# Kernel optimization log

Hardware: AMD Instinct MI355X
Metric: run time of the kernel (lower is better)

## Reference

```python
import jax, jax.numpy as jnp
import numpy as np

STRIDE = 4
N_LAYERS = 4
N_HEADS = 8
D_MODEL = 1024
D_FF = 4096
WINDOW = 400 // STRIDE      # lookback window (in folded frames)
LOOKFWD = 80 // STRIDE      # lookforward (in folded frames)
ROPE_BASE = 10000.0


def _layernorm(x, scale, bias, eps=1e-5):
    mu = jnp.mean(x, axis=-1, keepdims=True)
    var = jnp.mean(jnp.square(x - mu), axis=-1, keepdims=True)
    return (x - mu) * jax.lax.rsqrt(var + eps) * scale + bias


def _rope(x):
    # x: [B, H, S, Dh]
    B, H, S, Dh = x.shape
    half = Dh // 2
    inv_freq = 1.0 / (ROPE_BASE ** (jnp.arange(half, dtype=jnp.float32) / half))
    ang = jnp.arange(S, dtype=jnp.float32)[:, None] * inv_freq[None, :]  # [S, half]
    cos = jnp.cos(ang).astype(x.dtype)
    sin = jnp.sin(ang).astype(x.dtype)
    x1, x2 = x[..., :half], x[..., half:]
    return jnp.concatenate([x1 * cos - x2 * sin, x1 * sin + x2 * cos], axis=-1)


def setup_inputs() -> dict:
    key = jax.random.key(0)
    ks = jax.random.split(key, 32)
    B, T, C = 4, 4096, 512
    L, D, F = N_LAYERS, D_MODEL, D_FF
    s = 0.02
    inp = {
        'x': jax.random.normal(ks[0], (B, T, C), dtype=jnp.float32),
        'x_lengths': jax.random.randint(ks[1], (B,), 0, T + 1, dtype=jnp.int64 if jax.config.jax_enable_x64 else jnp.int32),
        'Wp': jax.random.normal(ks[2], (C * STRIDE, D), dtype=jnp.float32) * s,
        'bp': jnp.zeros((D,), jnp.float32),
        'ln1_s': jnp.ones((L, D), jnp.float32), 'ln1_b': jnp.zeros((L, D), jnp.float32),
        'Wq': jax.random.normal(ks[3], (L, D, D), jnp.float32) * s, 'bq': jnp.zeros((L, D), jnp.float32),
        'Wk': jax.random.normal(ks[4], (L, D, D), jnp.float32) * s, 'bk': jnp.zeros((L, D), jnp.float32),
        'Wv': jax.random.normal(ks[5], (L, D, D), jnp.float32) * s, 'bv': jnp.zeros((L, D), jnp.float32),
        'Wo': jax.random.normal(ks[6], (L, D, D), jnp.float32) * s, 'bo': jnp.zeros((L, D), jnp.float32),
        'ln2_s': jnp.ones((L, D), jnp.float32), 'ln2_b': jnp.zeros((L, D), jnp.float32),
        'W1': jax.random.normal(ks[7], (L, D, F), jnp.float32) * s, 'b1': jnp.zeros((L, F), jnp.float32),
        'W2': jax.random.normal(ks[8], (L, F, D), jnp.float32) * s, 'b2': jnp.zeros((L, D), jnp.float32),
        'lnf_s': jnp.ones((D,), jnp.float32), 'lnf_b': jnp.zeros((D,), jnp.float32),
    }
    return inp


def reference(x, x_lengths, Wp, bp, ln1_s, ln1_b, Wq, bq, Wk, bk, Wv, bv, Wo, bo,
              ln2_s, ln2_b, W1, b1, W2, b2, lnf_s, lnf_b):
    B, T, C = x.shape
    S = T // STRIDE
    H, Dh = N_HEADS, D_MODEL // N_HEADS
    # stride-fold + input projection
    xf = x[:, :S * STRIDE].reshape(B, S, C * STRIDE)
    h = xf @ Wp + bp                                  # [B, S, D]
    lens = x_lengths // STRIDE
    pad = (jnp.arange(S)[None, :] < lens[:, None])    # [B, S] valid-key mask
    h = h * pad[:, :, None].astype(h.dtype)
    # sliding-window causal-with-lookforward mask + key padding
    i = jnp.arange(S)[:, None]
    j = jnp.arange(S)[None, :]
    win = (j - i <= LOOKFWD) & (i - j < WINDOW)       # [S, S]
    allowed = win[None, None] & pad[:, None, None, :] # [B, 1, S, S]
    bias = jnp.where(allowed, 0.0, -1e9).astype(h.dtype)
    scale = 1.0 / jnp.sqrt(jnp.asarray(Dh, h.dtype))
    for l in range(N_LAYERS):
        # --- pre-LN RoPE windowed attention ---
        y = _layernorm(h, ln1_s[l], ln1_b[l])
        q = (y @ Wq[l] + bq[l]).reshape(B, S, H, Dh).transpose(0, 2, 1, 3)
        k = (y @ Wk[l] + bk[l]).reshape(B, S, H, Dh).transpose(0, 2, 1, 3)
        v = (y @ Wv[l] + bv[l]).reshape(B, S, H, Dh).transpose(0, 2, 1, 3)
        q, k = _rope(q), _rope(k)
        scores = jnp.einsum('bhqe,bhke->bhqk', q, k) * scale + bias
        attn = jax.nn.softmax(scores, axis=-1)
        ctx = jnp.einsum('bhqk,bhke->bhqe', attn, v)
        ctx = ctx.transpose(0, 2, 1, 3).reshape(B, S, D_MODEL)
        h = h + ctx @ Wo[l] + bo[l]
        # --- pre-LN FFN (kernel_size=1 conv == linear), swish ---
        y = _layernorm(h, ln2_s[l], ln2_b[l])
        h = h + jax.nn.silu(y @ W1[l] + b1[l]) @ W2[l] + b2[l]
    return _layernorm(h, lnf_s, lnf_b)
```

## Files before the change

kernel.cpp:

```cpp
#include <hip/hip_runtime.h>
#include <hip/hip_bf16.h>
#include <math.h>

typedef __hip_bfloat16 bf16;
typedef __attribute__((ext_vector_type(8))) short short8;
typedef __attribute__((ext_vector_type(4))) float f32x4;

#define S_LEN 1024
#define BATCH 4
#define M_ROWS 4096
#define DMODEL 1024
#define DFF 4096
#define NHEAD 8
#define DHEAD 128
#define WIN 100
#define LFWD 20

__device__ __forceinline__ void gl_lds16(const void* g, void* l) {
    __builtin_amdgcn_global_load_lds(
        (const __attribute__((address_space(1))) void*)g,
        (__attribute__((address_space(3))) void*)l, 16, 0, 0);
}

__device__ __forceinline__ float bf2f(unsigned short u) {
    return __uint_as_float(((unsigned)u) << 16);
}

__device__ __forceinline__ int xcd_swz(int flat, int nb) {
    return (flat & 7) * (nb >> 3) + (flat >> 3);
}

template<typename TC>
__global__ __launch_bounds__(256)
void mfma_gemm(const bf16* __restrict__ A, const bf16* __restrict__ Bt,
               const float* __restrict__ bias, TC* __restrict__ C,
               int M, int N, int K, int act)
{
    __shared__ bf16 As[2][128 * 32];
    __shared__ bf16 Bs[2][128 * 32];
    const int gx = gridDim.x;
    const int nb = gx * gridDim.y;
    const int swz = xcd_swz(blockIdx.x + gx * blockIdx.y, nb);
    const int bn = (swz % gx) * 128;
    const int bm = (swz / gx) * 128;
    const int tid = threadIdx.x;
    const int w = tid >> 6, lane = tid & 63;
    const int wm = (w & 1) * 64, wn = (w >> 1) * 64;

    const int srow = w * 32 + (lane >> 2);
    const int selem = (lane & 3) * 8;
    const bf16* ga0 = A + (size_t)(bm + srow) * K + selem;
    const bf16* ga1 = ga0 + (size_t)16 * K;
    const bf16* gb0 = Bt + (size_t)(bn + srow) * K + selem;
    const bf16* gb1 = gb0 + (size_t)16 * K;
    const int l0 = (w * 32) * 32;
    const int l1 = (w * 32 + 16) * 32;

    f32x4 acc[4][4] = {};
    const int koff = (lane >> 4) * 8;
    const int fr = lane & 15;

    gl_lds16(ga0, As[0] + l0); gl_lds16(ga1, As[0] + l1);
    gl_lds16(gb0, Bs[0] + l0); gl_lds16(gb1, Bs[0] + l1);
    ga0 += 32; ga1 += 32; gb0 += 32; gb1 += 32;
    __syncthreads();

    const int nk = K >> 5;
    int cur = 0;
    for (int t = 0; t < nk; ++t) {
        if (t + 1 < nk) {
            bf16* a = As[cur ^ 1]; bf16* b = Bs[cur ^ 1];
            gl_lds16(ga0, a + l0); gl_lds16(ga1, a + l1);
            gl_lds16(gb0, b + l0); gl_lds16(gb1, b + l1);
            ga0 += 32; ga1 += 32; gb0 += 32; gb1 += 32;
        }
        short8 af[4], bfr[4];
#pragma unroll
        for (int i = 0; i < 4; ++i)
            af[i] = *(const short8*)(As[cur] + (wm + i * 16 + fr) * 32 + koff);
#pragma unroll
        for (int j = 0; j < 4; ++j)
            bfr[j] = *(const short8*)(Bs[cur] + (wn + j * 16 + fr) * 32 + koff);
#pragma unroll
        for (int i = 0; i < 4; ++i)
#pragma unroll
            for (int j = 0; j < 4; ++j)
                acc[i][j] = __builtin_amdgcn_mfma_f32_16x16x32_bf16(
                    af[i], bfr[j], acc[i][j], 0, 0, 0);
        __syncthreads();
        cur ^= 1;
    }

    const int cq = lane >> 4, cn = lane & 15;
#pragma unroll
    for (int i = 0; i < 4; ++i) {
#pragma unroll
        for (int r = 0; r < 4; ++r) {
            int row = bm + wm + i * 16 + cq * 4 + r;
#pragma unroll
            for (int j = 0; j < 4; ++j) {
                int col = bn + wn + j * 16 + cn;
                float v = acc[i][j][r] + bias[col];
                if (act) v = v / (1.0f + __expf(-v));
                C[(size_t)row * N + col] = (TC)v;
            }
        }
    }
}

__global__ __launch_bounds__(256)
void mfma_gemm_sk(const bf16* __restrict__ A, const bf16* __restrict__ Bt,
                  const float* __restrict__ bias, float* __restrict__ C,
                  const float* __restrict__ resid,
                  float* __restrict__ P0, float* __restrict__ P1, int prows0,
                  int M, int N, int K)
{
    __shared__ bf16 As[2][128 * 32];
    __shared__ bf16 Bs[2][128 * 32];
    const int gx = gridDim.x, gy = gridDim.y;
    const int nb = gx * gy * 2;
    const int swz = xcd_swz(blockIdx.x + gx * (blockIdx.y + gy * blockIdx.z), nb);
    const int bn = (swz % gx) * 128;
    const int bm = ((swz / gx) % gy) * 128;
    const int z  = swz / (gx * gy);
    const int khalf = K >> 1;
    const int kstart = z * khalf;
    const int tid = threadIdx.x;
    const int w = tid >> 6, lane = tid & 63;
    const int wm = (w & 1) * 64, wn = (w >> 1) * 64;

    const int srow = w * 32 + (lane >> 2);
    const int selem = (lane & 3) * 8;
    const bf16* ga0 = A + (size_t)(bm + srow) * K + kstart + selem;
    const bf16* ga1 = ga0 + (size_t)16 * K;
    const bf16* gb0 = Bt + (size_t)(bn + srow) * K + kstart + selem;
    const bf16* gb1 = gb0 + (size_t)16 * K;
    const int l0 = (w * 32) * 32;
    const int l1 = (w * 32 + 16) * 32;

    f32x4 acc[4][4] = {};
    const int koff = (lane >> 4) * 8;
    const int fr = lane & 15;

    gl_lds16(ga0, As[0] + l0); gl_lds16(ga1, As[0] + l1);
    gl_lds16(gb0, Bs[0] + l0); gl_lds16(gb1, Bs[0] + l1);
    ga0 += 32; ga1 += 32; gb0 += 32; gb1 += 32;
    __syncthreads();

    const int nk = khalf >> 5;
    int cur = 0;
    for (int t = 0; t < nk; ++t) {
        if (t + 1 < nk) {
            bf16* a = As[cur ^ 1]; bf16* b = Bs[cur ^ 1];
            gl_lds16(ga0, a + l0); gl_lds16(ga1, a + l1);
            gl_lds16(gb0, b + l0); gl_lds16(gb1, b + l1);
            ga0 += 32; ga1 += 32; gb0 += 32; gb1 += 32;
        }
        short8 af[4], bfr[4];
#pragma unroll
        for (int i = 0; i < 4; ++i)
            af[i] = *(const short8*)(As[cur] + (wm + i * 16 + fr) * 32 + koff);
#pragma unroll
        for (int j = 0; j < 4; ++j)
            bfr[j] = *(const short8*)(Bs[cur] + (wn + j * 16 + fr) * 32 + koff);
#pragma unroll
        for (int i = 0; i < 4; ++i)
#pragma unroll
            for (int j = 0; j < 4; ++j)
                acc[i][j] = __builtin_amdgcn_mfma_f32_16x16x32_bf16(
                    af[i], bfr[j], acc[i][j], 0, 0, 0);
        __syncthreads();
        cur ^= 1;
    }

    const int cq = lane >> 4, cn = lane & 15;
#pragma unroll
    for (int i = 0; i < 4; ++i) {
#pragma unroll
        for (int r = 0; r < 4; ++r) {
            int row = bm + wm + i * 16 + cq * 4 + r;
#pragma unroll
            for (int j = 0; j < 4; ++j) {
                int col = bn + wn + j * 16 + cn;
                float v = acc[i][j][r];
                if (z == 0) {
                    v += bias[col];
                    if (resid) v += resid[(size_t)row * N + col];
                    C[(size_t)row * N + col] = v;
                } else {
                    float* P = (row < prows0) ? (P0 + (size_t)row * N + col)
                                              : (P1 + (size_t)(row - prows0) * N + col);
                    *P = v;
                }
            }
        }
    }
}

__global__ void transpose_kernel(const float* __restrict__ W, bf16* __restrict__ Wt,
                                 int K, int N, int ld)
{
    __shared__ float t[32][33];
    const int n0 = blockIdx.x * 32, k0 = blockIdx.y * 32;
    const int tx = threadIdx.x & 31, ty = threadIdx.x >> 5;
#pragma unroll
    for (int i = 0; i < 32; i += 8)
        t[ty + i][tx] = W[(size_t)(k0 + ty + i) * ld + n0 + tx];
    __syncthreads();
#pragma unroll
    for (int i = 0; i < 32; i += 8)
        Wt[(size_t)(n0 + ty + i) * K + k0 + tx] = (bf16)t[tx][ty + i];
}

__global__ void vtrans_kernel(const bf16* __restrict__ qkv, bf16* __restrict__ vt)
{
    __shared__ bf16 t[32][33];
    const int bh = blockIdx.z;
    const int s0 = blockIdx.x * 32, d0 = blockIdx.y * 32;
    const int b = bh >> 3, h = bh & 7;
    const int tx = threadIdx.x & 31, ty = threadIdx.x >> 5;
#pragma unroll
    for (int i = 0; i < 32; i += 8)
        t[ty + i][tx] = qkv[(size_t)(b * S_LEN + s0 + ty + i) * 3072 + 2048
                            + h * DHEAD + d0 + tx];
    __syncthreads();
#pragma unroll
    for (int i = 0; i < 32; i += 8)
        vt[(size_t)(bh * DHEAD + d0 + ty + i) * 1024 + s0 + tx] = t[tx][ty + i];
}

__global__ void cvt_kernel(const float* __restrict__ s, bf16* __restrict__ d)
{
    size_t i = ((size_t)blockIdx.x * 256 + threadIdx.x) * 4;
    float4 v = *(const float4*)(s + i);
    d[i] = (bf16)v.x; d[i + 1] = (bf16)v.y; d[i + 2] = (bf16)v.z; d[i + 3] = (bf16)v.w;
}

__global__ void concat3_kernel(const float* __restrict__ a, const float* __restrict__ b,
                               const float* __restrict__ c, float* __restrict__ o)
{
    int i = blockIdx.x * 256 + threadIdx.x;
    o[i] = (i < 1024) ? a[i] : (i < 2048 ? b[i - 1024] : c[i - 2048]);
}

__global__ void pad_red_kernel(float* __restrict__ h, const float* __restrict__ P,
                               const int* __restrict__ xlen)
{
    int row = blockIdx.x;
    int b = row >> 10, s = row & 1023;
    int len = xlen[b] >> 2;
    size_t off = (size_t)row * DMODEL;
    if (s >= len) {
        for (int d = threadIdx.x; d < DMODEL; d += 256) h[off + d] = 0.0f;
    } else {
        for (int d = threadIdx.x; d < DMODEL; d += 256) h[off + d] += P[off + d];
    }
}

__global__ void reduce2_kernel(float* __restrict__ h, const float* __restrict__ P0,
                               const float* __restrict__ P1, int prows0)
{
    int row = blockIdx.x;
    const float* P = (row < prows0) ? (P0 + (size_t)row * DMODEL)
                                    : (P1 + (size_t)(row - prows0) * DMODEL);
    size_t off = (size_t)row * DMODEL;
#pragma unroll
    for (int t = 0; t < 4; ++t) {
        int d = threadIdx.x + 256 * t;
        h[off + d] += P[d];
    }
}

template<typename TO, bool RED>
__global__ void ln_kernel(float* __restrict__ x, const float* __restrict__ P0,
                          const float* __restrict__ sc, const float* __restrict__ bi,
                          TO* __restrict__ y)
{
    int row = blockIdx.x;
    float* xr = x + (size_t)row * DMODEL;
    const float* pr = RED ? (P0 + (size_t)row * DMODEL) : nullptr;
    float vals[4];
    float lsum = 0.0f, lsq = 0.0f;
#pragma unroll
    for (int t = 0; t < 4; ++t) {
        int d = threadIdx.x + 256 * t;
        float v = xr[d];
        if (RED) { v += pr[d]; xr[d] = v; }
        vals[t] = v; lsum += v; lsq += v * v;
    }
    for (int o = 32; o > 0; o >>= 1) {
        lsum += __shfl_down(lsum, o, 64);
        lsq  += __shfl_down(lsq,  o, 64);
    }
    __shared__ float s1[4], s2[4];
    int wv = threadIdx.x >> 6, ln = threadIdx.x & 63;
    if (ln == 0) { s1[wv] = lsum; s2[wv] = lsq; }
    __syncthreads();
    if (threadIdx.x == 0) {
        float a = s1[0] + s1[1] + s1[2] + s1[3];
        float b = s2[0] + s2[1] + s2[2] + s2[3];
        float mu = a * (1.0f / DMODEL);
        float var = b * (1.0f / DMODEL) - mu * mu;
        s1[0] = mu;
        s2[0] = rsqrtf(fmaxf(var, 0.0f) + 1e-5f);
    }
    __syncthreads();
    float mu = s1[0], inv = s2[0];
#pragma unroll
    for (int t = 0; t < 4; ++t) {
        int d = threadIdx.x + 256 * t;
        y[(size_t)row * DMODEL + d] = (TO)((vals[t] - mu) * inv * sc[d] + bi[d]);
    }
}

__global__ void rope_kernel(bf16* __restrict__ q, bf16* __restrict__ k, int stride)
{
    size_t idx = (size_t)blockIdx.x * 256 + threadIdx.x;
    int d = idx & 63;
    size_t rest = idx >> 6;
    int hh = rest & 7;
    int s = (rest >> 3) & 1023;
    size_t base = (rest >> 3) * stride + (size_t)hh * DHEAD;
    float inv = exp2f((float)d * -0.20762050593045235f);
    float ang = (float)s * inv;
    float c, si;
    __sincosf(ang, &si, &c);
    {
        float x1 = (float)q[base + d], x2 = (float)q[base + 64 + d];
        q[base + d]      = (bf16)(x1 * c - x2 * si);
        q[base + 64 + d] = (bf16)(x1 * si + x2 * c);
    }
    {
        float x1 = (float)k[base + d], x2 = (float)k[base + 64 + d];
        k[base + d]      = (bf16)(x1 * c - x2 * si);
        k[base + 64 + d] = (bf16)(x1 * si + x2 * c);
    }
}

__global__ void vmean_part(const bf16* __restrict__ v, float* __restrict__ part,
                           int stride)
{
    int g = blockIdx.x;
    int chunk = g & 31;
    int bh = g >> 5;
    int b = bh >> 3, hh = bh & 7;
    int d = threadIdx.x;
    const bf16* base = v + ((size_t)(b * S_LEN + chunk * 32)) * stride
                         + hh * DHEAD + d;
    float acc = 0.0f;
#pragma unroll 4
    for (int s = 0; s < 32; ++s)
        acc += (float)base[(size_t)s * stride];
    part[((size_t)bh * 32 + chunk) * DHEAD + d] = acc;
}

__global__ void vmean_fin(const float* __restrict__ part, float* __restrict__ vmean)
{
    int bh = blockIdx.x;
    int d = threadIdx.x;
    float acc = 0.0f;
#pragma unroll
    for (int c = 0; c < 32; ++c)
        acc += part[((size_t)bh * 32 + c) * DHEAD + d];
    vmean[(size_t)bh * DHEAD + d] = acc * (1.0f / S_LEN);
}

__global__ __launch_bounds__(128)
void attn_mfma(const bf16* __restrict__ qkv, const bf16* __restrict__ vt_g,
               const float* __restrict__ vmean, const int* __restrict__ xlen,
               bf16* __restrict__ ctx)
{
    __shared__ bf16 KV[2][64 * 128];
    __shared__ bf16 P[2][16 * 192];

    const int qt = blockIdx.x;
    const int bh = blockIdx.y;
    const int b = bh >> 3, h = bh & 7;
    const int tid = threadIdx.x;
    const int w = tid >> 6, l = tid & 63;
    const int qlo = qt * 32;
    const int len = xlen[b] >> 2;

    int s0 = qlo - 128; if (s0 < 0) s0 = 0;
    const int jmax = qlo + 51;
    int k0t[3]; int nt = 0;
#pragma unroll
    for (int t = 0; t < 3; ++t) {
        int k0 = s0 + t * 64;
        if (k0 <= jmax && k0 < len) { k0t[nt] = k0; ++nt; }
    }

    const bf16* qbase = qkv + (size_t)(b * S_LEN) * 3072 + h * DHEAD;
    const bf16* kbase = qbase + DMODEL;

    short8 qa[4];
    {
        const bf16* qr = qbase + (size_t)(qlo + w * 16 + (l & 15)) * 3072 + (l >> 4) * 8;
#pragma unroll
        for (int kk = 0; kk < 4; ++kk)
            qa[kk] = *(const short8*)(qr + kk * 32);
    }

    auto stageK = [&](int k0, int buf) {
#pragma unroll
        for (int c = 0; c < 8; ++c) {
            int rl = w * 32 + c * 4 + (l >> 4);
            int sr = k0 + rl; if (sr > S_LEN - 1) sr = S_LEN - 1;
            int sc = ((l & 15) * 8) ^ ((rl & 7) << 3);
            gl_lds16(kbase + (size_t)sr * 3072 + sc,
                     &KV[buf][(w * 32 + c * 4) * 128]);
        }
    };
    auto stageV = [&](int k0, int buf) {
#pragma unroll
        for (int c = 0; c < 8; ++c) {
            int d = w * 64 + c * 8 + (l >> 3);
            int js = ((l & 7) * 8) ^ ((d & 7) << 3);
            int s = k0 + js; if (s > S_LEN - 8) s = S_LEN - 8;
            gl_lds16(vt_g + (size_t)(bh * 128 + d) * 1024 + s,
                     &KV[buf][(w * 64 + c * 8) * 64]);
        }
    };

    f32x4 sf[3][4] = {};

    auto sphase = [&](int t, int buf) {
#pragma unroll
        for (int jb = 0; jb < 4; ++jb) {
            int row = jb * 16 + (l & 15);
#pragma unroll
            for (int kk = 0; kk < 4; ++kk) {
                int kel = (kk * 32 + (l >> 4) * 8) ^ ((row & 7) << 3);
                short8 kf = *(const short8*)(&KV[buf][row * 128 + kel]);
                sf[t][jb] = __builtin_amdgcn_mfma_f32_16x16x32_bf16(
                    qa[kk], kf, sf[t][jb], 0, 0, 0);
            }
        }
    };

    if (nt > 0) stageK(k0t[0], 0);
    __syncthreads();
    if (nt > 1) stageK(k0t[1], 1);
    if (nt > 0) sphase(0, 0);
    __syncthreads();
    if (nt > 2) stageK(k0t[2], 0);
    if (nt > 1) sphase(1, 1);
    __syncthreads();
    if (nt > 2) sphase(2, 0);
    if (nt > 0) stageV(k0t[0], 1);

    const float scale = 0.088388347648318447f;
    float mr[4] = {-1e30f, -1e30f, -1e30f, -1e30f};
#pragma unroll
    for (int t = 0; t < 3; ++t) if (t < nt) {
#pragma unroll
        for (int jb = 0; jb < 4; ++jb) {
            int j = k0t[t] + jb * 16 + (l & 15);
            bool jok = (j < len);
#pragma unroll
            for (int r = 0; r < 4; ++r) {
                int i = qlo + w * 16 + ((l >> 4) << 2) + r;
                float v = sf[t][jb][r] * scale;
                bool ok = jok && (j - i <= LFWD) && (i - j < WIN);
                v = ok ? v : -1e30f;
                sf[t][jb][r] = v;
                mr[r] = fmaxf(mr[r], v);
            }
        }
    }
#pragma unroll
    for (int o = 1; o <= 8; o <<= 1)
#pragma unroll
        for (int r = 0; r < 4; ++r)
            mr[r] = fmaxf(mr[r], __shfl_xor(mr[r], o, 64));

    float lr[4] = {0.0f, 0.0f, 0.0f, 0.0f};
#pragma unroll
    for (int t = 0; t < 3; ++t) if (t < nt) {
#pragma unroll
        for (int jb = 0; jb < 4; ++jb) {
#pragma unroll
            for (int r = 0; r < 4; ++r) {
                int q = ((l >> 4) << 2) + r;
                int jrel = t * 64 + jb * 16 + (l & 15);
                float e = __expf(sf[t][jb][r] - mr[r]);
                lr[r] += e;
                P[w][q * 192 + (jrel ^ ((q & 7) << 3))] = (bf16)e;
            }
        }
    }
#pragma unroll
    for (int o = 1; o <= 8; o <<= 1)
#pragma unroll
        for (int r = 0; r < 4; ++r)
            lr[r] += __shfl_xor(lr[r], o, 64);
    float inv[4];
#pragma unroll
    for (int r = 0; r < 4; ++r) inv[r] = 1.0f / fmaxf(lr[r], 1e-30f);

    __syncthreads();

    f32x4 acc[8] = {};
    auto pv = [&](int ti, int buf) {
#pragma unroll
        for (int s32 = 0; s32 < 2; ++s32) {
            int q = l & 15;
            int jr8 = ti * 64 + s32 * 32 + (l >> 4) * 8;
            short8 pa = *(const short8*)(&P[w][q * 192 + (jr8 ^ ((q & 7) << 3))]);
#pragma unroll
            for (int db = 0; db < 8; ++db) {
                int d = db * 16 + (l & 15);
                int je = (s32 * 32 + (l >> 4) * 8) ^ ((d & 7) << 3);
                short8 vf = *(const short8*)(&KV[buf][d * 64 + je]);
                acc[db] = __builtin_amdgcn_mfma_f32_16x16x32_bf16(
                    pa, vf, acc[db], 0, 0, 0);
            }
        }
    };

    if (nt > 1) stageV(k0t[1], 0);
    if (nt > 0) pv(0, 1);
    __syncthreads();
    if (nt > 2) stageV(k0t[2], 1);
    if (nt > 1) pv(1, 0);
    __syncthreads();
    if (nt > 2) pv(2, 1);

    const float* vm = vmean + (size_t)bh * DHEAD;
    float vmr[8];
#pragma unroll
    for (int db = 0; db < 8; ++db) vmr[db] = vm[db * 16 + (l & 15)];
#pragma unroll
    for (int r = 0; r < 4; ++r) {
        int i = qlo + w * 16 + ((l >> 4) << 2) + r;
        bf16* crow = ctx + (size_t)(b * S_LEN + i) * DMODEL + h * DHEAD;
        bool em = mr[r] < -1e29f;
        float iv = inv[r];
#pragma unroll
        for (int db = 0; db < 8; ++db) {
            float v = em ? vmr[db] : acc[db][r] * iv;
            crow[db * 16 + (l & 15)] = (bf16)v;
        }
    }
}

extern "C" void kernel_launch(void* const* d_in, const int* in_sizes, int n_in,
                              void* d_out, int out_size, void* d_ws, size_t ws_size,
                              hipStream_t stream)
{
    const float* x      = (const float*)d_in[0];
    const int*   xlen   = (const int*)d_in[1];
    const float* Wp     = (const float*)d_in[2];
    const float* bp     = (const float*)d_in[3];
    const float* ln1_s  = (const float*)d_in[4];
    const float* ln1_b  = (const float*)d_in[5];
    const float* Wq     = (const float*)d_in[6];
    const float* bq     = (const float*)d_in[7];
    const float* Wk     = (const float*)d_in[8];
    const float* bk     = (const float*)d_in[9];
    const float* Wv     = (const float*)d_in[10];
    const float* bv     = (const float*)d_in[11];
    const float* Wo     = (const float*)d_in[12];
    const float* bo     = (const float*)d_in[13];
    const float* ln2_s  = (const float*)d_in[14];
    const float* ln2_b  = (const float*)d_in[15];
    const float* W1     = (const float*)d_in[16];
    const float* b1     = (const float*)d_in[17];
    const float* W2     = (const float*)d_in[18];
    const float* b2     = (const float*)d_in[19];
    const float* lnf_s  = (const float*)d_in[20];
    const float* lnf_b  = (const float*)d_in[21];
    (void)in_sizes; (void)n_in; (void)out_size; (void)ws_size;

    const size_t MD = (size_t)M_ROWS * DMODEL;
    float* h     = (float*)d_ws;
    bf16*  y     = (bf16*)(h + MD);
    float* yfP   = (float*)(h + MD);
    bf16*  U     = y + MD;
    bf16*  xb    = U;
    bf16*  qkv   = U;
    bf16*  mid   = U;
    float* UfP   = (float*)U;
    float* UfP2  = (float*)(U + 8 * 1024 * 1024);
    float* vmean = (float*)(U + 16 * 1024 * 1024);
    float* bqkv  = vmean + BATCH * NHEAD * DHEAD;
    bf16*  wt    = (bf16*)d_out;
    float* doP   = (float*)((char*)d_out + 8 * 1024 * 1024);
    float* vpart = doP;
    bf16*  vt_g  = (bf16*)d_out;
    const int QS = 3 * DMODEL;

    dim3 blk(256);
    dim3 gSK(DMODEL / 128, M_ROWS / 128, 2);

    cvt_kernel<<<(2 * MD) / (256 * 4), blk, 0, stream>>>(x, xb);
    transpose_kernel<<<dim3(DMODEL / 32, 2048 / 32), blk, 0, stream>>>(Wp, wt, 2048, DMODEL, DMODEL);
    mfma_gemm_sk<<<gSK, blk, 0, stream>>>(xb, wt, bp, h, nullptr,
                                          UfP2, nullptr, M_ROWS, M_ROWS, DMODEL, 2048);
    pad_red_kernel<<<M_ROWS, blk, 0, stream>>>(h, UfP2, xlen);

    for (int l = 0; l < 4; ++l) {
        const size_t wD  = (size_t)l * DMODEL * DMODEL;
        const size_t wF  = (size_t)l * DMODEL * DFF;
        const size_t wF2 = (size_t)l * DFF * DMODEL;
        const size_t vD  = (size_t)l * DMODEL;
        const size_t vF  = (size_t)l * DFF;

        ln_kernel<bf16, false><<<M_ROWS, blk, 0, stream>>>(h, nullptr,
                                                           ln1_s + vD, ln1_b + vD, y);

        transpose_kernel<<<dim3(32, 32), blk, 0, stream>>>(Wq + wD, wt, DMODEL, DMODEL, DMODEL);
        transpose_kernel<<<dim3(32, 32), blk, 0, stream>>>(Wk + wD, wt + MD / 4, DMODEL, DMODEL, DMODEL);
        transpose_kernel<<<dim3(32, 32), blk, 0, stream>>>(Wv + wD, wt + MD / 2, DMODEL, DMODEL, DMODEL);
        concat3_kernel<<<12, blk, 0, stream>>>(bq + vD, bk + vD, bv + vD, bqkv);
        mfma_gemm<bf16><<<dim3(3 * DMODEL / 128, M_ROWS / 128), blk, 0, stream>>>(
            y, wt, bqkv, qkv, M_ROWS, 3 * DMODEL, DMODEL, 0);

        bf16* qb = qkv;
        bf16* kb = qkv + DMODEL;
        bf16* vb = qkv + 2 * DMODEL;
        rope_kernel<<<(M_ROWS * NHEAD * 64) / 256, blk, 0, stream>>>(qb, kb, QS);
        vtrans_kernel<<<dim3(32, 4, 32), blk, 0, stream>>>(qkv, vt_g);
        vmean_part<<<BATCH * NHEAD * 32, dim3(DHEAD), 0, stream>>>(vb, vpart, QS);
        vmean_fin<<<BATCH * NHEAD, dim3(DHEAD), 0, stream>>>(vpart, vmean);
        attn_mfma<<<dim3(32, 32), dim3(128), 0, stream>>>(qkv, vt_g, vmean, xlen, y);

        transpose_kernel<<<dim3(32, 32), blk, 0, stream>>>(Wo + wD, wt, DMODEL, DMODEL, DMODEL);
        mfma_gemm_sk<<<gSK, blk, 0, stream>>>(y, wt, bo + vD, h, h,
                                              UfP, nullptr, M_ROWS, M_ROWS, DMODEL, 1024);

        ln_kernel<bf16, true><<<M_ROWS, blk, 0, stream>>>(h, UfP,
                                                          ln2_s + vD, ln2_b + vD, y);

        transpose_kernel<<<dim3(DFF / 32, DMODEL / 32), blk, 0, stream>>>(
            W1 + wF, wt, DMODEL, DFF, DFF);
        mfma_gemm<bf16><<<dim3(DFF / 128, M_ROWS / 128), blk, 0, stream>>>(
            y, wt, b1 + vF, mid, M_ROWS, DFF, DMODEL, 1);

        transpose_kernel<<<dim3(DMODEL / 32, DFF / 32), blk, 0, stream>>>(
            W2 + wF2, wt, DFF, DMODEL, DMODEL);
        mfma_gemm_sk<<<gSK, blk, 0, stream>>>(mid, wt, b2 + vD, h, h,
                                              yfP, doP, 2048, M_ROWS, DMODEL, DFF);
        reduce2_kernel<<<M_ROWS, blk, 0, stream>>>(h, yfP, doP, 2048);
    }

    ln_kernel<float, false><<<M_ROWS, blk, 0, stream>>>(h, nullptr, lnf_s, lnf_b,
                                                        (float*)d_out);
}
```

Baseline: 1.466 ms.

## Triple-buffer GEMM LDS staging with explicit vmcnt waits and barriers

Both MFMA GEMM kernels move from double-buffered to triple-buffered LDS tiles. Two K-tiles are kept in flight, and precise s_waitcnt vmcnt counts decide when a tile is ready, in place of a full __syncthreads after each step. This is meant to hide more global-load latency behind the MFMA work. The cost is 48KB of LDS per block, which may lower occupancy, plus two barriers per iteration, and the code relies on hand-counted vmcnt values being correct.

```diff
diff --git a/kernel.cpp b/kernel.cpp
--- a/kernel.cpp
+++ b/kernel.cpp
@@ -16,6 +16,8 @@
 #define WIN 100
 #define LFWD 20
 
+#define SCHED0 __builtin_amdgcn_sched_barrier(0)
+
 __device__ __forceinline__ void gl_lds16(const void* g, void* l) {
     __builtin_amdgcn_global_load_lds(
         (const __attribute__((address_space(1))) void*)g,
@@ -36,8 +38,8 @@
                const float* __restrict__ bias, TC* __restrict__ C,
                int M, int N, int K, int act)
 {
-    __shared__ bf16 As[2][128 * 32];
-    __shared__ bf16 Bs[2][128 * 32];
+    __shared__ bf16 As[3][128 * 32];
+    __shared__ bf16 Bs[3][128 * 32];
     const int gx = gridDim.x;
     const int nb = gx * gridDim.y;
     const int swz = xcd_swz(blockIdx.x + gx * blockIdx.y, nb);
@@ -60,35 +62,46 @@
     const int koff = (lane >> 4) * 8;
     const int fr = lane & 15;
 
-    gl_lds16(ga0, As[0] + l0); gl_lds16(ga1, As[0] + l1);
-    gl_lds16(gb0, Bs[0] + l0); gl_lds16(gb1, Bs[0] + l1);
-    ga0 += 32; ga1 += 32; gb0 += 32; gb1 += 32;
-    __syncthreads();
+    auto STAGE = [&](int t, int buf) {
+        gl_lds16(ga0 + t * 32, As[buf] + l0);
+        gl_lds16(ga1 + t * 32, As[buf] + l1);
+        gl_lds16(gb0 + t * 32, Bs[buf] + l0);
+        gl_lds16(gb1 + t * 32, Bs[buf] + l1);
+    };
 
     const int nk = K >> 5;
-    int cur = 0;
+    STAGE(0, 0);
+    if (nk > 1) STAGE(1, 1);
+    if (nk > 2) STAGE(2, 2);
+
     for (int t = 0; t < nk; ++t) {
-        if (t + 1 < nk) {
-            bf16* a = As[cur ^ 1]; bf16* b = Bs[cur ^ 1];
-            gl_lds16(ga0, a + l0); gl_lds16(ga1, a + l1);
-            gl_lds16(gb0, b + l0); gl_lds16(gb1, b + l1);
-            ga0 += 32; ga1 += 32; gb0 += 32; gb1 += 32;
-        }
+        const int ahead = nk - 1 - t;
+        if (ahead >= 2)      asm volatile("s_waitcnt vmcnt(8)" ::: "memory");
+        else if (ahead == 1) asm volatile("s_waitcnt vmcnt(4)" ::: "memory");
+        else                 asm volatile("s_waitcnt vmcnt(0)" ::: "memory");
+        SCHED0;
+        __builtin_amdgcn_s_barrier();
+        SCHED0;
+        const bf16* Ac = As[t % 3];
+        const bf16* Bc = Bs[t % 3];
         short8 af[4], bfr[4];
 #pragma unroll
         for (int i = 0; i < 4; ++i)
-            af[i] = *(const short8*)(As[cur] + (wm + i * 16 + fr) * 32 + koff);
+            af[i] = *(const short8*)(Ac + (wm + i * 16 + fr) * 32 + koff);
 #pragma unroll
         for (int j = 0; j < 4; ++j)
-            bfr[j] = *(const short8*)(Bs[cur] + (wn + j * 16 + fr) * 32 + koff);
+            bfr[j] = *(const short8*)(Bc + (wn + j * 16 + fr) * 32 + koff);
 #pragma unroll
         for (int i = 0; i < 4; ++i)
 #pragma unroll
             for (int j = 0; j < 4; ++j)
                 acc[i][j] = __builtin_amdgcn_mfma_f32_16x16x32_bf16(
                     af[i], bfr[j], acc[i][j], 0, 0, 0);
-        __syncthreads();
-        cur ^= 1;
+        asm volatile("s_waitcnt lgkmcnt(0)" ::: "memory");
+        SCHED0;
+        __builtin_amdgcn_s_barrier();
+        SCHED0;
+        if (t + 3 < nk) STAGE(t + 3, t % 3);
     }
 
     const int cq = lane >> 4, cn = lane & 15;
@@ -115,8 +128,8 @@
                   float* __restrict__ P0, float* __restrict__ P1, int prows0,
                   int M, int N, int K)
 {
-    __shared__ bf16 As[2][128 * 32];
-    __shared__ bf16 Bs[2][128 * 32];
+    __shared__ bf16 As[3][128 * 32];
+    __shared__ bf16 Bs[3][128 * 32];
     const int gx = gridDim.x, gy = gridDim.y;
     const int nb = gx * gy * 2;
     const int swz = xcd_swz(blockIdx.x + gx * (blockIdx.y + gy * blockIdx.z), nb);
@@ -142,35 +155,46 @@
     const int koff = (lane >> 4) * 8;
     const int fr = lane & 15;
 
-    gl_lds16(ga0, As[0] + l0); gl_lds16(ga1, As[0] + l1);
-    gl_lds16(gb0, Bs[0] + l0); gl_lds16(gb1, Bs[0] + l1);
-    ga0 += 32; ga1 += 32; gb0 += 32; gb1 += 32;
-    __syncthreads();
+    auto STAGE = [&](int t, int buf) {
+        gl_lds16(ga0 + t * 32, As[buf] + l0);
+        gl_lds16(ga1 + t * 32, As[buf] + l1);
+        gl_lds16(gb0 + t * 32, Bs[buf] + l0);
+        gl_lds16(gb1 + t * 32, Bs[buf] + l1);
+    };
 
     const int nk = khalf >> 5;
-    int cur = 0;
+    STAGE(0, 0);
+    if (nk > 1) STAGE(1, 1);
+    if (nk > 2) STAGE(2, 2);
+
     for (int t = 0; t < nk; ++t) {
-        if (t + 1 < nk) {
-            bf16* a = As[cur ^ 1]; bf16* b = Bs[cur ^ 1];
-            gl_lds16(ga0, a + l0); gl_lds16(ga1, a + l1);
-            gl_lds16(gb0, b + l0); gl_lds16(gb1, b + l1);
-            ga0 += 32; ga1 += 32; gb0 += 32; gb1 += 32;
-        }
+        const int ahead = nk - 1 - t;
+        if (ahead >= 2)      asm volatile("s_waitcnt vmcnt(8)" ::: "memory");
+        else if (ahead == 1) asm volatile("s_waitcnt vmcnt(4)" ::: "memory");
+        else                 asm volatile("s_waitcnt vmcnt(0)" ::: "memory");
+        SCHED0;
+        __builtin_amdgcn_s_barrier();
+        SCHED0;
+        const bf16* Ac = As[t % 3];
+        const bf16* Bc = Bs[t % 3];
         short8 af[4], bfr[4];
 #pragma unroll
         for (int i = 0; i < 4; ++i)
-            af[i] = *(const short8*)(As[cur] + (wm + i * 16 + fr) * 32 + koff);
+            af[i] = *(const short8*)(Ac + (wm + i * 16 + fr) * 32 + koff);
 #pragma unroll
         for (int j = 0; j < 4; ++j)
-            bfr[j] = *(const short8*)(Bs[cur] + (wn + j * 16 + fr) * 32 + koff);
+            bfr[j] = *(const short8*)(Bc + (wn + j * 16 + fr) * 32 + koff);
 #pragma unroll
         for (int i = 0; i < 4; ++i)
 #pragma unroll
             for (int j = 0; j < 4; ++j)
                 acc[i][j] = __builtin_amdgcn_mfma_f32_16x16x32_bf16(
                     af[i], bfr[j], acc[i][j], 0, 0, 0);
-        __syncthreads();
-        cur ^= 1;
+        asm volatile("s_waitcnt lgkmcnt(0)" ::: "memory");
+        SCHED0;
+        __builtin_amdgcn_s_barrier();
+        SCHED0;
+        if (t + 3 < nk) STAGE(t + 3, t % 3);
     }
 
     const int cq = lane >> 4, cn = lane & 15;
```

Result: no change. 1.451 ms (-1.0%).
